# Kernel optimization log

Hardware: AMD Instinct MI355X
Metric: run time of the kernel (lower is better)

Reference implementation:

```python
import jax, jax.numpy as jnp
import numpy as np
import math

D_MODEL = 2048
N_HEADS = 16
HEAD_DIM = D_MODEL // N_HEADS


def setup_inputs() -> dict:
    key = jax.random.key(0)
    k1, k2, k3, k4 = jax.random.split(key, 4)
    bs, seq = 2, 2048
    x = jax.random.normal(k1, (bs, seq, D_MODEL), dtype=jnp.float32)
    # torch nn.Linear weights are [out, in]; y = x @ W.T
    scale_q = 1.0 / math.sqrt(D_MODEL)
    Wq = jax.random.uniform(k2, (D_MODEL, D_MODEL), jnp.float32, -scale_q, scale_q)
    Wkv = jax.random.uniform(k3, (2 * HEAD_DIM, D_MODEL), jnp.float32, -scale_q, scale_q)
    Wo = jax.random.uniform(k4, (D_MODEL, D_MODEL), jnp.float32, -scale_q, scale_q)
    return {"x": x, "Wq": Wq, "Wkv": Wkv, "Wo": Wo}


def reference(x, Wq, Wkv, Wo):
    bs, seq, _ = x.shape
    q = x @ Wq.T                      # [b, s, d_model]
    kv = x @ Wkv.T                    # [b, s, 2*head_dim]
    k, v = jnp.split(kv, 2, axis=-1)  # each [b, s, head_dim] (single shared KV head)
    q = q.reshape(bs, seq, N_HEADS, HEAD_DIM).transpose(0, 2, 1, 3)  # [b, h, s, d]
    # MQA: broadcast shared K/V across heads via einsum (no explicit expand)
    attn = jnp.einsum("bhqd,bkd->bhqk", q, k) / math.sqrt(HEAD_DIM)  # [b, h, s, s]
    causal = jnp.tril(jnp.ones((seq, seq), dtype=bool))
    attn = jnp.where(causal[None, None], attn, jnp.float32(-1e9))
    attn = jax.nn.softmax(attn, axis=-1)
    out = jnp.einsum("bhqk,bkd->bhqd", attn, v)                      # [b, h, s, d]
    out = out.transpose(0, 2, 1, 3).reshape(bs, seq, D_MODEL)
    return out @ Wo.T
```

## Files before the change

### kernel.cpp

```cpp
#include <hip/hip_runtime.h>
#include <hip/hip_bf16.h>

typedef __attribute__((ext_vector_type(8))) short bf16x8;
typedef __attribute__((ext_vector_type(4))) float f32x4;
typedef __attribute__((ext_vector_type(16))) float f32x16;
typedef __attribute__((ext_vector_type(4))) ushort u16x4;

#define AS1 __attribute__((address_space(1)))
#define AS3 __attribute__((address_space(3)))

static __device__ __forceinline__ ushort f2b(float f) {
    union { float f; unsigned u; } v;
    v.f = f;
    unsigned r = v.u + 0x7FFF + ((v.u >> 16) & 1);
    return (ushort)(r >> 16);
}

__global__ __launch_bounds__(256) void cvt_all(const float* __restrict__ x,
                                               const float* __restrict__ Wq,
                                               const float* __restrict__ Wkv,
                                               const float* __restrict__ Wo,
                                               ushort* __restrict__ xb,
                                               ushort* __restrict__ wqkvb,
                                               ushort* __restrict__ wob)
{
    int i = blockIdx.x * blockDim.x + threadIdx.x;
    const int stride = gridDim.x * blockDim.x;
    for (; i < 4325376; i += stride) {
        const float4* src; ushort4* dst; int j;
        if (i < 2097152)      { src = (const float4*)x;   dst = (ushort4*)xb;              j = i; }
        else if (i < 3145728) { src = (const float4*)Wq;  dst = (ushort4*)wqkvb;           j = i - 2097152; }
        else if (i < 3276800) { src = (const float4*)Wkv; dst = (ushort4*)wqkvb + 1048576; j = i - 3145728; }
        else                  { src = (const float4*)Wo;  dst = (ushort4*)wob;             j = i - 3276800; }
        float4 v = src[j];
        ushort4 o; o.x = f2b(v.x); o.y = f2b(v.y); o.z = f2b(v.z); o.w = f2b(v.w);
        dst[j] = o;
    }
}

template<bool F32OUT>
__global__ __launch_bounds__(512) void gemm_bt(const ushort* __restrict__ A,
                                               const ushort* __restrict__ B,
                                               void* __restrict__ Cv,
                                               int M, int N, int K)
{
    __shared__ ushort As[2][128 * 32];
    __shared__ ushort Bs[2][128 * 32];
    const int tid  = threadIdx.x;
    const int lane = tid & 63;
    const int wid  = tid >> 6;
    const int l15  = lane & 15;
    const int lg   = lane >> 4;
    const int nwg8 = gridDim.x >> 3;
    const int kblk = blockIdx.x;
    const int swz  = (kblk & 7) * nwg8 + (kblk >> 3);
    const int nx   = N >> 7;
    const int brow = (swz / nx) * 128;
    const int bcol = (swz % nx) * 128;
    const int wr = wid >> 2, wc = wid & 3;

    f32x4 acc[4][2] = {};

    auto stage = [&](int bi, int k0) {
        const ushort* Ap = A + (size_t)brow * K + k0;
        const ushort* Bp = B + (size_t)bcol * K + k0;
        const int r   = tid >> 2;
        const int sgc = (tid & 3) ^ ((r >> 1) & 3);
        __builtin_amdgcn_global_load_lds(
            (const AS1 void*)(Ap + (size_t)r * K + sgc * 8),
            (AS3 void*)(&As[bi][wid * 512]), 16, 0, 0);
        __builtin_amdgcn_global_load_lds(
            (const AS1 void*)(Bp + (size_t)r * K + sgc * 8),
            (AS3 void*)(&Bs[bi][wid * 512]), 16, 0, 0);
    };

    stage(0, 0);
    __syncthreads();
    int cur = 0;

    for (int k0 = 0; k0 < K; k0 += 32) {
        if (k0 + 32 < K) stage(cur ^ 1, k0 + 32);

        bf16x8 af[4], bfr[2];
#pragma unroll
        for (int m = 0; m < 4; ++m) {
            int row = wr * 64 + m * 16 + l15;
            int slot = lg ^ ((row >> 1) & 3);
            af[m] = *(const bf16x8*)(&As[cur][row * 32 + slot * 8]);
        }
#pragma unroll
        for (int n = 0; n < 2; ++n) {
            int row = wc * 32 + n * 16 + l15;
            int slot = lg ^ ((row >> 1) & 3);
            bfr[n] = *(const bf16x8*)(&Bs[cur][row * 32 + slot * 8]);
        }
#pragma unroll
        for (int m = 0; m < 4; ++m)
#pragma unroll
            for (int n = 0; n < 2; ++n)
                acc[m][n] = __builtin_amdgcn_mfma_f32_16x16x32_bf16(af[m], bfr[n], acc[m][n], 0, 0, 0);

        __syncthreads();
        cur ^= 1;
    }

#pragma unroll
    for (int m = 0; m < 4; ++m)
#pragma unroll
        for (int n = 0; n < 2; ++n) {
            int row0 = brow + wr * 64 + m * 16 + lg * 4;
            int col  = bcol + wc * 32 + n * 16 + l15;
#pragma unroll
            for (int j = 0; j < 4; ++j) {
                float v = acc[m][n][j];
                if (F32OUT)
                    ((float*)Cv)[(size_t)(row0 + j) * N + col] = v;
                else
                    ((ushort*)Cv)[(size_t)(row0 + j) * N + col] = f2b(v);
            }
        }
}

__global__ __launch_bounds__(512) void gemm_qkv(const ushort* __restrict__ A,
                                                const ushort* __restrict__ B,
                                                ushort* __restrict__ Cq,
                                                ushort* __restrict__ Ckv,
                                                ushort* __restrict__ Vt,
                                                int M, int K)
{
    __shared__ ushort As[2][128 * 32];
    __shared__ ushort Bs[2][128 * 32];
    const int tid  = threadIdx.x;
    const int lane = tid & 63;
    const int wid  = tid >> 6;
    const int l15  = lane & 15;
    const int lg   = lane >> 4;
    const int nwg8 = gridDim.x >> 3;
    const int kblk = blockIdx.x;
    const int swz  = (kblk & 7) * nwg8 + (kblk >> 3);
    const int brow = (swz / 18) * 128;
    const int bcol = (swz % 18) * 128;
    const int wr = wid >> 2, wc = wid & 3;

    f32x4 acc[4][2] = {};

    auto stage = [&](int bi, int k0) {
        const ushort* Ap = A + (size_t)brow * K + k0;
        const ushort* Bp = B + (size_t)bcol * K + k0;
        const int r   = tid >> 2;
        const int sgc = (tid & 3) ^ ((r >> 1) & 3);
        __builtin_amdgcn_global_load_lds(
            (const AS1 void*)(Ap + (size_t)r * K + sgc * 8),
            (AS3 void*)(&As[bi][wid * 512]), 16, 0, 0);
        __builtin_amdgcn_global_load_lds(
            (const AS1 void*)(Bp + (size_t)r * K + sgc * 8),
            (AS3 void*)(&Bs[bi][wid * 512]), 16, 0, 0);
    };

    stage(0, 0);
    __syncthreads();
    int cur = 0;

    for (int k0 = 0; k0 < K; k0 += 32) {
        if (k0 + 32 < K) stage(cur ^ 1, k0 + 32);

        bf16x8 af[4], bfr[2];
#pragma unroll
        for (int m = 0; m < 4; ++m) {
            int row = wr * 64 + m * 16 + l15;
            int slot = lg ^ ((row >> 1) & 3);
            af[m] = *(const bf16x8*)(&As[cur][row * 32 + slot * 8]);
        }
#pragma unroll
        for (int n = 0; n < 2; ++n) {
            int row = wc * 32 + n * 16 + l15;
            int slot = lg ^ ((row >> 1) & 3);
            bfr[n] = *(const bf16x8*)(&Bs[cur][row * 32 + slot * 8]);
        }
#pragma unroll
        for (int m = 0; m < 4; ++m)
#pragma unroll
            for (int n = 0; n < 2; ++n)
                acc[m][n] = __builtin_amdgcn_mfma_f32_16x16x32_bf16(af[m], bfr[n], acc[m][n], 0, 0, 0);

        __syncthreads();
        cur ^= 1;
    }

    const bool toK = (bcol == 2048);
    const bool toV = (bcol == 2176);
#pragma unroll
    for (int m = 0; m < 4; ++m)
#pragma unroll
        for (int n = 0; n < 2; ++n) {
            int row0 = brow + wr * 64 + m * 16 + lg * 4;
            int col  = bcol + wc * 32 + n * 16 + l15;
#pragma unroll
            for (int j = 0; j < 4; ++j) {
                float v = acc[m][n][j];
                int row = row0 + j;
                if (toV) {
                    int d = col - 2176;
                    int bb = row >> 11, s = row & 2047;
                    Vt[((size_t)(bb * 128 + d)) * 2048 + s] = f2b(v);
                } else if (toK) {
                    Ckv[(size_t)row * 256 + (col - 2048)] = f2b(v);
                } else {
                    Cq[(size_t)row * 2048 + col] = f2b(v);
                }
            }
        }
}

__global__ __launch_bounds__(256, 2) void mqa_attn12(const ushort* __restrict__ Q,
                                                     const ushort* __restrict__ KV,
                                                     const ushort* __restrict__ Vt,
                                                     ushort* __restrict__ O)
{
    const int tid = threadIdx.x, lane = tid & 63, wid = tid >> 6;
    const int c31 = lane & 31, H = lane >> 5;
    const int bid = blockIdx.x;
    const int a  = bid & 31;
    const int hp = (bid >> 5) & 7;
    const int b  = bid >> 8;
    const int h  = hp * 2 + (wid >> 1);
    const int p  = wid & 1;

    __shared__ __align__(16) ushort SMEM[32768];

    const ushort* KVb = KV + (size_t)b * 2048 * 256;
    const ushort* Vtb = Vt + (size_t)b * 128 * 2048;
    const float C2 = 0.12751763f;
    const float mC = 32.0f * C2;

    auto stageK = [&](int buf, int par, int t) {
        ushort* dst = SMEM + (buf * 2 + par) * 4096;
        const int kvb = t * 32;
#pragma unroll
        for (int i = 0; i < 8; ++i) {
            int G = i * 64 + lane;
            int r = G >> 4, gc = G & 15;
            int sgc = gc ^ (r & 15);
            __builtin_amdgcn_global_load_lds(
                (const AS1 void*)(KVb + (size_t)(kvb + r) * 256 + sgc * 8),
                (AS3 void*)(dst + i * 512), 16, 0, 0);
        }
    };
    auto stageV = [&](int buf, int par, int t) {
        ushort* dst = SMEM + 16384 + (buf * 2 + par) * 4096;
        const int kvb = t * 32;
#pragma unroll
        for (int i = 0; i < 8; ++i) {
            int G = i * 64 + lane;
            int g = G >> 3, s = G & 7;
            int u = s ^ (g & 7);
            int r = 2 * g + (u & 1);
            int cc = u >> 1;
            __builtin_amdgcn_global_load_lds(
                (const AS1 void*)(Vtb + (size_t)r * 2048 + kvb + cc * 8),
                (AS3 void*)(dst + G * 8), 16, 0, 0);
        }
    };

#pragma unroll 1
    for (int phase = 0; phase < 2; ++phase) {
        const int tile  = phase ? (63 - a) : a;
        const int qtile = tile * 32;
        const int U = tile + 1;
        const int S = (U + 1) >> 1;
        const size_t qrow = (size_t)(b * 2048 + qtile + c31);

        bf16x8 qf[8];
#pragma unroll
        for (int dk = 0; dk < 8; ++dk)
            qf[dk] = *(const bf16x8*)(Q + qrow * 2048 + h * 128 + dk * 16 + H * 8);

        float l_run = 0.f;
        f32x16 of[4];
#pragma unroll
        for (int dt = 0; dt < 4; ++dt)
#pragma unroll
            for (int r = 0; r < 16; ++r) of[dt][r] = 0.f;

        {
            int t = p;
            if (t < U) { if (wid < 2) stageK(0, p, t); else stageV(0, p, t); }
        }
        __syncthreads();

#pragma unroll 1
        for (int s = 0; s < S; ++s) {
            if (s + 1 < S) {
                int tn = 2 * (s + 1) + p;
                if (tn < U) { if (wid < 2) stageK((s + 1) & 1, p, tn); else stageV((s + 1) & 1, p, tn); }
            }
            const int t = 2 * s + p;
            if (t < U) {
                const ushort* Kb = SMEM + ((s & 1) * 2 + p) * 4096;
                const ushort* Vb = SMEM + 16384 + ((s & 1) * 2 + p) * 4096;
                const bool maskt = (t == tile);

                f32x16 sg = {0,0,0,0,0,0,0,0,0,0,0,0,0,0,0,0};
                __builtin_amdgcn_s_setprio(1);
#pragma unroll
                for (int dk = 0; dk < 8; ++dk) {
                    bf16x8 kf = *(const bf16x8*)(Kb + c31 * 128 + ((dk * 16 + H * 8) ^ ((c31 & 15) << 3)));
                    sg = __builtin_amdgcn_mfma_f32_32x32x16_bf16(kf, qf[dk], sg, 0, 0, 0);
                }
                __builtin_amdgcn_s_setprio(0);

                float e[16];
#pragma unroll
                for (int r = 0; r < 16; ++r) {
                    float v = sg[r];
                    if (maskt) {
                        int crow = (r & 3) + 8 * (r >> 2) + 4 * H;
                        if (crow > c31) v = -1e30f;
                    }
                    e[r] = __builtin_amdgcn_exp2f(__builtin_fmaf(v, C2, -mC));
                }
                float rsum = 0.f;
#pragma unroll
                for (int r = 0; r < 16; ++r) rsum += e[r];
                rsum += __shfl_xor(rsum, 32);
                l_run += rsum;

                unsigned pk[8];
#pragma unroll
                for (int i = 0; i < 8; ++i)
                    asm("v_cvt_pk_bf16_f32 %0, %1, %2" : "=v"(pk[i]) : "v"(e[2 * i]), "v"(e[2 * i + 1]));
                asm("v_permlane32_swap_b32 %0, %1" : "+v"(pk[0]), "+v"(pk[2]));
                asm("v_permlane32_swap_b32 %0, %1" : "+v"(pk[1]), "+v"(pk[3]));
                asm("v_permlane32_swap_b32 %0, %1" : "+v"(pk[4]), "+v"(pk[6]));
                asm("v_permlane32_swap_b32 %0, %1" : "+v"(pk[5]), "+v"(pk[7]));
                union { unsigned u[4]; bf16x8 v; } P0, P1;
                P0.u[0] = pk[0]; P0.u[1] = pk[1]; P0.u[2] = pk[2]; P0.u[3] = pk[3];
                P1.u[0] = pk[4]; P1.u[1] = pk[5]; P1.u[2] = pk[6]; P1.u[3] = pk[7];

                __builtin_amdgcn_s_setprio(1);
#pragma unroll
                for (int dt = 0; dt < 4; ++dt) {
                    int g  = dt * 16 + (c31 >> 1);
                    int sw = g & 7;
                    int b0 = c31 & 1;
                    int s0 = (2 * H + b0) ^ sw;
                    int s1 = (4 + 2 * H + b0) ^ sw;
                    bf16x8 v0 = *(const bf16x8*)(Vb + (g * 8 + s0) * 8);
                    bf16x8 v1 = *(const bf16x8*)(Vb + (g * 8 + s1) * 8);
                    of[dt] = __builtin_amdgcn_mfma_f32_32x32x16_bf16(v0, P0.v, of[dt], 0, 0, 0);
                    of[dt] = __builtin_amdgcn_mfma_f32_32x32x16_bf16(v1, P1.v, of[dt], 0, 0, 0);
                }
                __builtin_amdgcn_s_setprio(0);
            }
            __syncthreads();
        }

        float* mlb = (float*)SMEM;
        if (H == 0) mlb[wid * 32 + c31] = l_run;
        __syncthreads();
        {
            float lo = mlb[(wid ^ 1) * 32 + c31];
            float inv = 1.0f / (l_run + lo);
            float* ob = (float*)(SMEM + 512) + (wid >> 1) * 4096;
            if (p == 1) {
#pragma unroll
                for (int dt = 0; dt < 4; ++dt)
#pragma unroll
                    for (int rq = 0; rq < 4; ++rq) {
                        f32x4 w;
#pragma unroll
                        for (int j = 0; j < 4; ++j) w[j] = of[dt][rq * 4 + j];
                        *(f32x4*)(ob + ((dt * 4 + rq) * 64 + lane) * 4) = w;
                    }
            }
            __syncthreads();
            if (p == 0) {
                ushort* Orow = O + qrow * 2048 + h * 128;
#pragma unroll
                for (int dt = 0; dt < 4; ++dt)
#pragma unroll
                    for (int rq = 0; rq < 4; ++rq) {
                        f32x4 r4 = *(const f32x4*)(ob + ((dt * 4 + rq) * 64 + lane) * 4);
                        u16x4 o4;
#pragma unroll
                        for (int j = 0; j < 4; ++j)
                            o4[j] = f2b((of[dt][rq * 4 + j] + r4[j]) * inv);
                        int d0 = dt * 32 + rq * 8 + 4 * H;
                        *(u16x4*)(Orow + d0) = o4;
                    }
            }
        }
        __syncthreads();
    }
}

extern "C" void kernel_launch(void* const* d_in, const int* in_sizes, int n_in,
                              void* d_out, int out_size, void* d_ws, size_t ws_size,
                              hipStream_t stream) {
    const float* x   = (const float*)d_in[0];
    const float* Wq  = (const float*)d_in[1];
    const float* Wkv = (const float*)d_in[2];
    const float* Wo  = (const float*)d_in[3];

    char* ws = (char*)d_ws;
    ushort* xb    = (ushort*)(ws);
    ushort* wqkvb = (ushort*)(ws + 16777216);
    ushort* wob   = (ushort*)(ws + 35651584);
    ushort* qb    = (ushort*)(ws + 44040192);
    ushort* kvb   = (ushort*)(ws + 60817408);
    ushort* vtb   = (ushort*)(ws + 62914560);
    ushort* aob   = xb;

    cvt_all<<<2048, 256, 0, stream>>>(x, Wq, Wkv, Wo, xb, wqkvb, wob);

    gemm_qkv<<<576, 512, 0, stream>>>(xb, wqkvb, qb, kvb, vtb, 4096, 2048);
    mqa_attn12<<<512, 256, 0, stream>>>(qb, kvb, vtb, aob);
    gemm_bt<true><<<512, 512, 0, stream>>>(aob, wob, d_out, 4096, 2048, 2048);
}
```

Measured before the change: 171.7 us.

## Restructure output GEMM to 4 waves with 64x64 warp tiles and BK=64

The output projection GEMM now runs 256 threads instead of 512, so each wave computes a 64x64 sub-tile rather than 64x32. The K step doubles to 64, and the LDS swizzle is changed to match. This raises MFMA work per LDS fragment load and halves the number of barriers per K. In exchange it uses more accumulator registers and twice the LDS per block, and has fewer waves per block to hide latency.

```diff
diff --git a/kernel.cpp b/kernel.cpp
--- a/kernel.cpp
+++ b/kernel.cpp
@@ -39,13 +39,13 @@
 }
 
 template<bool F32OUT>
-__global__ __launch_bounds__(512) void gemm_bt(const ushort* __restrict__ A,
+__global__ __launch_bounds__(256) void gemm_bt(const ushort* __restrict__ A,
                                                const ushort* __restrict__ B,
                                                void* __restrict__ Cv,
                                                int M, int N, int K)
 {
-    __shared__ ushort As[2][128 * 32];
-    __shared__ ushort Bs[2][128 * 32];
+    __shared__ ushort As[2][128 * 64];
+    __shared__ ushort Bs[2][128 * 64];
     const int tid  = threadIdx.x;
     const int lane = tid & 63;
     const int wid  = tid >> 6;
@@ -57,48 +57,61 @@
     const int nx   = N >> 7;
     const int brow = (swz / nx) * 128;
     const int bcol = (swz % nx) * 128;
-    const int wr = wid >> 2, wc = wid & 3;
-
-    f32x4 acc[4][2] = {};
+    const int wr = wid >> 1, wc = wid & 1;
+
+    f32x4 acc[4][4] = {};
 
     auto stage = [&](int bi, int k0) {
         const ushort* Ap = A + (size_t)brow * K + k0;
         const ushort* Bp = B + (size_t)bcol * K + k0;
-        const int r   = tid >> 2;
-        const int sgc = (tid & 3) ^ ((r >> 1) & 3);
-        __builtin_amdgcn_global_load_lds(
-            (const AS1 void*)(Ap + (size_t)r * K + sgc * 8),
-            (AS3 void*)(&As[bi][wid * 512]), 16, 0, 0);
-        __builtin_amdgcn_global_load_lds(
-            (const AS1 void*)(Bp + (size_t)r * K + sgc * 8),
-            (AS3 void*)(&Bs[bi][wid * 512]), 16, 0, 0);
+#pragma unroll
+        for (int j = 0; j < 4; ++j) {
+            const int G = j * 256 + tid;
+            const int r = G >> 3;
+            const int s = (G & 7) ^ (r & 7);
+            const int dc = (j * 256 + (wid << 6)) * 8;
+            __builtin_amdgcn_global_load_lds(
+                (const AS1 void*)(Ap + (size_t)r * K + s * 8),
+                (AS3 void*)(&As[bi][dc]), 16, 0, 0);
+            __builtin_amdgcn_global_load_lds(
+                (const AS1 void*)(Bp + (size_t)r * K + s * 8),
+                (AS3 void*)(&Bs[bi][dc]), 16, 0, 0);
+        }
     };
 
     stage(0, 0);
     __syncthreads();
     int cur = 0;
 
-    for (int k0 = 0; k0 < K; k0 += 32) {
-        if (k0 + 32 < K) stage(cur ^ 1, k0 + 32);
-
-        bf16x8 af[4], bfr[2];
+    for (int k0 = 0; k0 < K; k0 += 64) {
+        if (k0 + 64 < K) stage(cur ^ 1, k0 + 64);
+
+        bf16x8 af[4][2], bfr[4][2];
 #pragma unroll
         for (int m = 0; m < 4; ++m) {
             int row = wr * 64 + m * 16 + l15;
-            int slot = lg ^ ((row >> 1) & 3);
-            af[m] = *(const bf16x8*)(&As[cur][row * 32 + slot * 8]);
-        }
-#pragma unroll
-        for (int n = 0; n < 2; ++n) {
-            int row = wc * 32 + n * 16 + l15;
-            int slot = lg ^ ((row >> 1) & 3);
-            bfr[n] = *(const bf16x8*)(&Bs[cur][row * 32 + slot * 8]);
+#pragma unroll
+            for (int kh = 0; kh < 2; ++kh) {
+                int sl = (kh * 4 + lg) ^ (row & 7);
+                af[m][kh] = *(const bf16x8*)(&As[cur][row * 64 + sl * 8]);
+            }
+        }
+#pragma unroll
+        for (int n = 0; n < 4; ++n) {
+            int row = wc * 64 + n * 16 + l15;
+#pragma unroll
+            for (int kh = 0; kh < 2; ++kh) {
+                int sl = (kh * 4 + lg) ^ (row & 7);
+                bfr[n][kh] = *(const bf16x8*)(&Bs[cur][row * 64 + sl * 8]);
+            }
         }
 #pragma unroll
         for (int m = 0; m < 4; ++m)
 #pragma unroll
-            for (int n = 0; n < 2; ++n)
-                acc[m][n] = __builtin_amdgcn_mfma_f32_16x16x32_bf16(af[m], bfr[n], acc[m][n], 0, 0, 0);
+            for (int n = 0; n < 4; ++n) {
+                acc[m][n] = __builtin_amdgcn_mfma_f32_16x16x32_bf16(af[m][0], bfr[n][0], acc[m][n], 0, 0, 0);
+                acc[m][n] = __builtin_amdgcn_mfma_f32_16x16x32_bf16(af[m][1], bfr[n][1], acc[m][n], 0, 0, 0);
+            }
 
         __syncthreads();
         cur ^= 1;
@@ -107,9 +120,9 @@
 #pragma unroll
     for (int m = 0; m < 4; ++m)
 #pragma unroll
-        for (int n = 0; n < 2; ++n) {
+        for (int n = 0; n < 4; ++n) {
             int row0 = brow + wr * 64 + m * 16 + lg * 4;
-            int col  = bcol + wc * 32 + n * 16 + l15;
+            int col  = bcol + wc * 64 + n * 16 + l15;
 #pragma unroll
             for (int j = 0; j < 4; ++j) {
                 float v = acc[m][n][j];
@@ -415,5 +428,5 @@
 
     gemm_qkv<<<576, 512, 0, stream>>>(xb, wqkvb, qb, kvb, vtb, 4096, 2048);
     mqa_attn12<<<512, 256, 0, stream>>>(qb, kvb, vtb, aob);
-    gemm_bt<true><<<512, 512, 0, stream>>>(aob, wob, d_out, 4096, 2048, 2048);
-}
+    gemm_bt<true><<<512, 256, 0, stream>>>(aob, wob, d_out, 4096, 2048, 2048);
+}
```

Result: no change. 168.4 us (-1.9%).
